# Kernel optimization log

Hardware: AMD Instinct MI355X
Metric: run time of the kernel (lower is better)

Reference implementation:

```python
import jax, jax.numpy as jnp
import numpy as np
from jax import lax

TAU = 0.25
N_TIMESTEPS = 12
OUTPUT_TICKS = 4
INPUT_DIM = 1024
HIDDEN = 1024
OUTPUT_DIM = 1024
CLEANUP = 512
BATCH = 1024
W_SD = 0.1


def setup_inputs() -> dict:
    key = jax.random.key(0)
    ks = jax.random.split(key, 6)
    inputs = jax.random.normal(ks[0], (BATCH, N_TIMESTEPS, INPUT_DIM), dtype=jnp.float32)
    w_oh = W_SD * jax.random.normal(ks[1], (INPUT_DIM, HIDDEN), dtype=jnp.float32)
    w_hp = W_SD * jax.random.normal(ks[2], (HIDDEN, OUTPUT_DIM), dtype=jnp.float32)
    w_pp = W_SD * jax.random.normal(ks[3], (OUTPUT_DIM, OUTPUT_DIM), dtype=jnp.float32)
    w_pc = W_SD * jax.random.normal(ks[4], (OUTPUT_DIM, CLEANUP), dtype=jnp.float32)
    w_cp = W_SD * jax.random.normal(ks[5], (CLEANUP, OUTPUT_DIM), dtype=jnp.float32)
    bias_h = jnp.zeros((HIDDEN,), jnp.float32)
    bias_p = jnp.zeros((OUTPUT_DIM,), jnp.float32)
    bias_c = jnp.zeros((CLEANUP,), jnp.float32)
    return {"inputs": inputs, "w_oh": w_oh, "w_hp": w_hp, "w_pp": w_pp,
            "w_pc": w_pc, "w_cp": w_cp, "bias_h": bias_h, "bias_p": bias_p,
            "bias_c": bias_c}


def reference(inputs, w_oh, w_hp, w_pp, w_pc, w_cp, bias_h, bias_p, bias_c):
    B = inputs.shape[0]
    act = jax.nn.sigmoid
    # time-major input stream: step t consumes o_input[:, t-1, :]
    x = jnp.swapaxes(inputs, 0, 1)  # [T, B, I]

    in_h0 = jnp.zeros((B, HIDDEN), jnp.float32)
    in_p0 = jnp.zeros((B, OUTPUT_DIM), jnp.float32)
    in_c0 = jnp.zeros((B, CLEANUP), jnp.float32)
    carry0 = (in_h0, in_p0, in_c0, in_h0 + 0.5, in_p0 + 0.5, in_c0 + 0.5)

    def step(carry, o_t):
        in_h, in_p, in_c, a_h, a_p, a_c = carry
        # leaky-integrator blends; hp/pp/cp/pc all use PREVIOUS step activations
        h = TAU * (o_t @ w_oh + bias_h) + (1.0 - TAU) * in_h
        p = TAU * (a_h @ w_hp + a_p @ w_pp + a_c @ w_cp + bias_p) + (1.0 - TAU) * in_p
        c = TAU * (a_p @ w_pc + bias_c) + (1.0 - TAU) * in_c
        a_p_new = act(p)
        new_carry = (h, p, c, act(h), a_p_new, act(c))
        return new_carry, a_p_new

    _, act_p_seq = lax.scan(step, carry0, x)  # [T, B, OUTPUT_DIM]
    return act_p_seq[-OUTPUT_TICKS:]  # [OUTPUT_TICKS, B, OUTPUT_DIM]
```

## Files before the change

kernel.cpp:

```cpp
#include <hip/hip_runtime.h>
#include <cstdint>
#include <cstddef>


typedef _Float16 half8 __attribute__((ext_vector_type(8)));
typedef float floatx4 __attribute__((ext_vector_type(4)));

__device__ __forceinline__ void async_cp16(const void* g, void* l) {
  __builtin_amdgcn_global_load_lds(
      (const __attribute__((address_space(1))) void*)g,
      (__attribute__((address_space(3))) void*)l, 16, 0, 0);
}

__device__ __forceinline__ float sigmoidf_(float x) {
  return 1.f / (1.f + __expf(-x));
}

__global__ __launch_bounds__(256) void k_transpose(
    const float* __restrict__ src, int K, int N,
    _Float16* __restrict__ dst, int dst_ld, int k_off) {
  __shared__ float tile[64][65];
  const int k0 = blockIdx.y * 64, n0 = blockIdx.x * 64;
  const int tx = threadIdx.x & 63, ty = threadIdx.x >> 6;
#pragma unroll
  for (int j = 0; j < 16; ++j) {
    int kr = j * 4 + ty;
    tile[kr][tx] = src[(size_t)(k0 + kr) * N + n0 + tx];
  }
  __syncthreads();
#pragma unroll
  for (int j = 0; j < 16; ++j) {
    int nr = j * 4 + ty;
    dst[(size_t)(n0 + nr) * dst_ld + k_off + k0 + tx] = (_Float16)tile[tx][nr];
  }
}

__global__ __launch_bounds__(256) void k_pack_frag(
    const float* __restrict__ src, int N, _Float16* __restrict__ dst,
    int kStride, int kOffChunks) {
  __shared__ float tile[64][65];
  const int k0 = blockIdx.y * 64, n0 = blockIdx.x * 64;
  const int tx = threadIdx.x & 63, ty = threadIdx.x >> 6;
#pragma unroll
  for (int jj = 0; jj < 16; ++jj) {
    int kr = jj * 4 + ty;
    tile[kr][tx] = src[(size_t)(k0 + kr) * N + n0 + tx];
  }
  __syncthreads();
  const int j = threadIdx.x >> 6, lane = threadIdx.x & 63;
  const int r16 = lane & 15, quad = lane >> 4;
#pragma unroll
  for (int c = 0; c < 2; ++c) {
    half8 v;
#pragma unroll
    for (int u = 0; u < 8; ++u)
      v[u] = (_Float16)tile[c * 32 + quad * 8 + u][j * 16 + r16];
    const int kcG = kOffChunks + blockIdx.y * 2 + c;
    *(half8*)(dst + ((size_t)(blockIdx.x * kStride + kcG) * 4 + j) * 512 +
              lane * 8) = v;
  }
}

__global__ __launch_bounds__(256) void k_prep(
    const float* __restrict__ x, _Float16* __restrict__ U,
    _Float16* __restrict__ AH0, _Float16* __restrict__ AP0,
    _Float16* __restrict__ AC0, float* __restrict__ Pst,
    float* __restrict__ Cst) {
  const int id = blockIdx.x * 256 + threadIdx.x;
  const int b = id >> 10, i = id & 1023;
  const float* xb = x + (size_t)b * 12 * 1024 + i;
  float g = 0.f;
#pragma unroll
  for (int t = 0; t < 11; ++t) {
    g = xb[t * 1024] + 0.75f * g;
    U[(size_t)t * 1048576 + id] = (_Float16)g;
  }
  AH0[id] = (_Float16)0.5f;
  AP0[id] = (_Float16)0.5f;
  Pst[id] = 0.f;
  if (i < 512) {
    const int cid = b * 512 + i;
    AC0[cid] = (_Float16)0.5f;
    Cst[cid] = 0.f;
  }
}

__global__ __launch_bounds__(64) void k_gemm_big(
    const _Float16* __restrict__ A, const _Float16* __restrict__ B,
    const float* __restrict__ bias, _Float16* __restrict__ dst, int mode) {
  __shared__ __align__(16) _Float16 sA[2 * 4096];
  __shared__ __align__(16) _Float16 sB[2 * 4096];
  const int lane = threadIdx.x;
  const int mBase = blockIdx.y * 64, nBase = blockIdx.x * 64;
  const int r16 = lane & 15, quad = lane >> 4, mrow = lane >> 3;
  const int gsw = ((lane & 7) ^ (mrow & 7)) * 8;
  const floatx4 zero = {0.f, 0.f, 0.f, 0.f};
  floatx4 acc[4][4];
#pragma unroll
  for (int i = 0; i < 4; ++i)
#pragma unroll
    for (int j = 0; j < 4; ++j) acc[i][j] = zero;

  const _Float16* Abase = A + (size_t)(mBase + mrow) * 1024 + gsw;
  const _Float16* Bbase = B + (size_t)(nBase + mrow) * 1024 + gsw;

  auto stage = [&](int kt, int buf) {
    const int k0 = kt << 6;
#pragma unroll
    for (int q = 0; q < 8; ++q)
      async_cp16(Abase + (size_t)q * 8192 + k0, sA + buf * 4096 + q * 512);
#pragma unroll
    for (int q = 0; q < 8; ++q)
      async_cp16(Bbase + (size_t)q * 8192 + k0, sB + buf * 4096 + q * 512);
  };

  stage(0, 0);
  for (int kt = 0; kt < 16; ++kt) {
    if (kt + 1 < 16) {
      stage(kt + 1, (kt + 1) & 1);
      asm volatile("s_waitcnt vmcnt(16)" ::: "memory");
    } else {
      asm volatile("s_waitcnt vmcnt(0)" ::: "memory");
    }
    const _Float16* sa = sA + (kt & 1) * 4096;
    const _Float16* sb = sB + (kt & 1) * 4096;
#pragma unroll
    for (int kk = 0; kk < 2; ++kk) {
      const int sw = ((kk * 4 + quad) ^ (r16 & 7)) * 8;
      half8 af[4], bf[4];
#pragma unroll
      for (int i = 0; i < 4; ++i) af[i] = *(const half8*)&sa[(i * 16 + r16) * 64 + sw];
#pragma unroll
      for (int j = 0; j < 4; ++j) bf[j] = *(const half8*)&sb[(j * 16 + r16) * 64 + sw];
#pragma unroll
      for (int i = 0; i < 4; ++i)
#pragma unroll
        for (int j = 0; j < 4; ++j)
          acc[i][j] =
              __builtin_amdgcn_mfma_f32_16x16x32_f16(af[i], bf[j], acc[i][j], 0, 0, 0);
    }
  }

  if (mode == 0) {
    const int tm1 = mBase >> 10;
    const float beta = 1.f - __powf(0.75f, (float)(tm1 + 1));
    _Float16* o = dst + (size_t)(mBase + 1024) * 1024;
#pragma unroll
    for (int i = 0; i < 4; ++i)
#pragma unroll
      for (int j = 0; j < 4; ++j) {
        const int n = nBase + j * 16 + r16;
#pragma unroll
        for (int r = 0; r < 4; ++r) {
          const int row = i * 16 + quad * 4 + r;
          const float h = 0.25f * acc[i][j][r] + beta * bias[n];
          o[(size_t)row * 1024 + n] = (_Float16)sigmoidf_(h);
        }
      }
  } else {
    _Float16* o = dst + (size_t)mBase * 1024;
#pragma unroll
    for (int i = 0; i < 4; ++i)
#pragma unroll
      for (int j = 0; j < 4; ++j) {
        const int n = nBase + j * 16 + r16;
#pragma unroll
        for (int r = 0; r < 4; ++r) {
          const int row = i * 16 + quad * 4 + r;
          o[(size_t)row * 1024 + n] = (_Float16)(0.25f * (acc[i][j][r] + bias[n]));
        }
      }
  }
}

__global__ __launch_bounds__(256, 3) void k_step(
    const _Float16* __restrict__ Qt, const _Float16* __restrict__ APc,
    const _Float16* __restrict__ ACc, _Float16* __restrict__ APn,
    _Float16* __restrict__ ACn, const _Float16* __restrict__ Wrf,
    const _Float16* __restrict__ Wcf, const float* __restrict__ bias_c,
    float* __restrict__ Pst, float* __restrict__ Cst,
    float* __restrict__ out_t) {
  __shared__ float red[4][2][4][4][64];
  const int lane = threadIdx.x & 63, w = threadIdx.x >> 6;
  const int r16 = lane & 15, quad = lane >> 4;
  const int blk = blockIdx.x;
  const bool isP = blk < 512;
  int mBase, nt;
  if (isP) {
    mBase = (blk >> 4) * 32;
    nt = blk & 15;
  } else {
    const int b = blk - 512;
    mBase = (b >> 3) * 32;
    nt = b & 7;
  }
  const int nBase = nt * 64;
  const floatx4 zero = {0.f, 0.f, 0.f, 0.f};
  floatx4 acc[2][4];
#pragma unroll
  for (int i = 0; i < 2; ++i)
#pragma unroll
    for (int j = 0; j < 4; ++j) acc[i][j] = zero;

  half8 abuf[3][2], bbuf[3][4];
  auto MM = [&](half8* af, half8* bf) {
#pragma unroll
    for (int i = 0; i < 2; ++i)
#pragma unroll
      for (int j = 0; j < 4; ++j)
        acc[i][j] = __builtin_amdgcn_mfma_f32_16x16x32_f16(af[i], bf[j],
                                                           acc[i][j], 0, 0, 0);
  };

  if (isP) {
    const int kcBase = w * 12;
    auto LD = [&](half8* af, half8* bf, int c) {
      const int kc = kcBase + c;
      const int kg = kc * 32;
      if (kc < 32) {
#pragma unroll
        for (int i = 0; i < 2; ++i)
          af[i] = *(const half8*)(APc + (size_t)(mBase + i * 16 + r16) * 1024 +
                                  kg + quad * 8);
      } else {
#pragma unroll
        for (int i = 0; i < 2; ++i)
          af[i] = *(const half8*)(ACc + (size_t)(mBase + i * 16 + r16) * 512 +
                                  (kg - 1024) + quad * 8);
      }
      const _Float16* wp = Wrf + (size_t)(nt * 48 + kc) * 2048 + lane * 8;
#pragma unroll
      for (int j = 0; j < 4; ++j) bf[j] = *(const half8*)(wp + j * 512);
    };
    LD(abuf[0], bbuf[0], 0);
    LD(abuf[1], bbuf[1], 1);
#pragma unroll
    for (int c = 0; c < 12; ++c) {
      if (c + 2 < 12) LD(abuf[(c + 2) % 3], bbuf[(c + 2) % 3], c + 2);
      MM(abuf[c % 3], bbuf[c % 3]);
    }
  } else {
    const int kcBase = w * 8;
    auto LD = [&](half8* af, half8* bf, int c) {
      const int kc = kcBase + c;
      const int kg = kc * 32;
#pragma unroll
      for (int i = 0; i < 2; ++i)
        af[i] = *(const half8*)(APc + (size_t)(mBase + i * 16 + r16) * 1024 +
                                kg + quad * 8);
      const _Float16* wp = Wcf + (size_t)(nt * 32 + kc) * 2048 + lane * 8;
#pragma unroll
      for (int j = 0; j < 4; ++j) bf[j] = *(const half8*)(wp + j * 512);
    };
    LD(abuf[0], bbuf[0], 0);
    LD(abuf[1], bbuf[1], 1);
#pragma unroll
    for (int c = 0; c < 8; ++c) {
      if (c + 2 < 8) LD(abuf[(c + 2) % 3], bbuf[(c + 2) % 3], c + 2);
      MM(abuf[c % 3], bbuf[c % 3]);
    }
  }

#pragma unroll
  for (int i = 0; i < 2; ++i)
#pragma unroll
    for (int j = 0; j < 4; ++j)
#pragma unroll
      for (int r = 0; r < 4; ++r) red[w][i][j][r][lane] = acc[i][j][r];
  __syncthreads();

  if (isP) {
#pragma unroll
    for (int i = 0; i < 2; ++i) {
      const int n = nBase + w * 16 + r16;
#pragma unroll
      for (int r = 0; r < 4; ++r) {
        const float v = red[0][i][w][r][lane] + red[1][i][w][r][lane] +
                        red[2][i][w][r][lane] + red[3][i][w][r][lane];
        const int b = mBase + i * 16 + quad * 4 + r;
        const size_t o = (size_t)b * 1024 + n;
        const float pn = 0.25f * v + (float)Qt[o] + 0.75f * Pst[o];
        Pst[o] = pn;
        const float a = sigmoidf_(pn);
        APn[o] = (_Float16)a;
        if (out_t) out_t[o] = a;
      }
    }
  } else {
#pragma unroll
    for (int i = 0; i < 2; ++i) {
      const int n = nBase + w * 16 + r16;
#pragma unroll
      for (int r = 0; r < 4; ++r) {
        const float v = red[0][i][w][r][lane] + red[1][i][w][r][lane] +
                        red[2][i][w][r][lane] + red[3][i][w][r][lane];
        const int b = mBase + i * 16 + quad * 4 + r;
        const size_t o = (size_t)b * 512 + n;
        const float cn = 0.25f * (v + bias_c[n]) + 0.75f * Cst[o];
        Cst[o] = cn;
        ACn[o] = (_Float16)sigmoidf_(cn);
      }
    }
  }
}

extern "C" void kernel_launch(void* const* d_in, const int* in_sizes, int n_in,
                              void* d_out, int out_size, void* d_ws,
                              size_t ws_size, hipStream_t stream) {
  const float* x      = (const float*)d_in[0];
  const float* w_oh   = (const float*)d_in[1];
  const float* w_hp   = (const float*)d_in[2];
  const float* w_pp   = (const float*)d_in[3];
  const float* w_pc   = (const float*)d_in[4];
  const float* w_cp   = (const float*)d_in[5];
  const float* bias_h = (const float*)d_in[6];
  const float* bias_p = (const float*)d_in[7];
  const float* bias_c = (const float*)d_in[8];
  float* out = (float*)d_out;

  uint8_t* p = (uint8_t*)d_ws;
  _Float16* Wrf  = (_Float16*)p; p += (size_t)1024 * 1536 * 2;
  _Float16* Wcf  = (_Float16*)p; p += (size_t)512 * 1024 * 2;
  _Float16* WohT = (_Float16*)p; p += (size_t)1024 * 1024 * 2;
  _Float16* Whp  = (_Float16*)p; p += (size_t)1024 * 1024 * 2;
  _Float16* U    = (_Float16*)p; p += (size_t)11 * 1048576 * 2;
  _Float16* AH   = (_Float16*)p; p += (size_t)12 * 1048576 * 2;
  _Float16* Q    = (_Float16*)p; p += (size_t)12 * 1048576 * 2;
  _Float16* AP0  = (_Float16*)p; p += (size_t)1048576 * 2;
  _Float16* AP1  = (_Float16*)p; p += (size_t)1048576 * 2;
  _Float16* AC0  = (_Float16*)p; p += (size_t)512 * 1024 * 2;
  _Float16* AC1  = (_Float16*)p; p += (size_t)512 * 1024 * 2;
  float* Pst = (float*)p; p += (size_t)1048576 * 4;
  float* Cst = (float*)p; p += (size_t)512 * 1024 * 4;

  const dim3 blk256(256);
  k_transpose<<<dim3(16, 16), blk256, 0, stream>>>(w_oh, 1024, 1024, WohT, 1024, 0);
  k_transpose<<<dim3(16, 16), blk256, 0, stream>>>(w_hp, 1024, 1024, Whp, 1024, 0);
  k_pack_frag<<<dim3(16, 16), blk256, 0, stream>>>(w_pp, 1024, Wrf, 48, 0);
  k_pack_frag<<<dim3(16, 8),  blk256, 0, stream>>>(w_cp, 1024, Wrf, 48, 32);
  k_pack_frag<<<dim3(8, 16),  blk256, 0, stream>>>(w_pc, 512, Wcf, 32, 0);
  k_prep<<<4096, blk256, 0, stream>>>(x, U, AH, AP0, AC0, Pst, Cst);
  k_gemm_big<<<dim3(16, 176), dim3(64), 0, stream>>>(U, WohT, bias_h, AH, 0);
  k_gemm_big<<<dim3(16, 192), dim3(64), 0, stream>>>(AH, Whp, bias_p, Q, 1);
  for (int t = 0; t < 12; ++t) {
    const _Float16* APc = (t & 1) ? AP1 : AP0;
    _Float16* APn       = (t & 1) ? AP0 : AP1;
    const _Float16* ACc = (t & 1) ? AC1 : AC0;
    _Float16* ACn       = (t & 1) ? AC0 : AC1;
    float* ot = (t >= 8) ? out + (size_t)(t - 8) * 1048576 : (float*)nullptr;
    k_step<<<dim3(768), blk256, 0, stream>>>(Q + (size_t)t * 1048576, APc,
                                             ACc, APn, ACn, Wrf, Wcf, bias_c,
                                             Pst, Cst, ot);
  }
}
```

Before: 435.9 us.

## Use 128x128 four-wave tiles in big GEMM with cooperative LDS staging

The batched input and hidden-to-output GEMMs move from a single-wave 64x64 tile to a 256-thread block computing a 128x128 tile, with four waves sharing the A and B tiles in LDS. This halves global loads per output and cuts block count fourfold. The double-buffered async prefetch is dropped for a single buffer with a full vmcnt wait and two barriers per k-step, so load latency is no longer hidden behind MFMA work.

```diff
diff --git a/kernel.cpp b/kernel.cpp
--- a/kernel.cpp
+++ b/kernel.cpp
@@ -85,15 +85,19 @@
   }
 }
 
-__global__ __launch_bounds__(64) void k_gemm_big(
+__global__ __launch_bounds__(256, 3) void k_gemm_big(
     const _Float16* __restrict__ A, const _Float16* __restrict__ B,
     const float* __restrict__ bias, _Float16* __restrict__ dst, int mode) {
-  __shared__ __align__(16) _Float16 sA[2 * 4096];
-  __shared__ __align__(16) _Float16 sB[2 * 4096];
-  const int lane = threadIdx.x;
-  const int mBase = blockIdx.y * 64, nBase = blockIdx.x * 64;
-  const int r16 = lane & 15, quad = lane >> 4, mrow = lane >> 3;
-  const int gsw = ((lane & 7) ^ (mrow & 7)) * 8;
+  __shared__ __align__(16) _Float16 sA[128 * 64];
+  __shared__ __align__(16) _Float16 sB[128 * 64];
+  const int tid = threadIdx.x;
+  const int lane = tid & 63, w = tid >> 6;
+  const int mBase = blockIdx.y * 128, nBase = blockIdx.x * 128;
+  const int r16 = lane & 15, quad = lane >> 4;
+  const int lrow = lane >> 3;
+  const int gsw = ((lane & 7) ^ lrow) * 8;
+  const int wr = w >> 1, wc = w & 1;
+
   const floatx4 zero = {0.f, 0.f, 0.f, 0.f};
   floatx4 acc[4][4];
 #pragma unroll
@@ -101,44 +105,41 @@
 #pragma unroll
     for (int j = 0; j < 4; ++j) acc[i][j] = zero;
 
-  const _Float16* Abase = A + (size_t)(mBase + mrow) * 1024 + gsw;
-  const _Float16* Bbase = B + (size_t)(nBase + mrow) * 1024 + gsw;
-
-  auto stage = [&](int kt, int buf) {
+  const _Float16* Abase = A + (size_t)(mBase + w * 32 + lrow) * 1024 + gsw;
+  const _Float16* Bbase = B + (size_t)(nBase + w * 32 + lrow) * 1024 + gsw;
+  _Float16* sAw = sA + (w * 32) * 64;
+  _Float16* sBw = sB + (w * 32) * 64;
+  const _Float16* sa = sA + (size_t)wr * 64 * 64;
+  const _Float16* sb = sB + (size_t)wc * 64 * 64;
+
+  for (int kt = 0; kt < 16; ++kt) {
     const int k0 = kt << 6;
 #pragma unroll
-    for (int q = 0; q < 8; ++q)
-      async_cp16(Abase + (size_t)q * 8192 + k0, sA + buf * 4096 + q * 512);
-#pragma unroll
-    for (int q = 0; q < 8; ++q)
-      async_cp16(Bbase + (size_t)q * 8192 + k0, sB + buf * 4096 + q * 512);
-  };
-
-  stage(0, 0);
-  for (int kt = 0; kt < 16; ++kt) {
-    if (kt + 1 < 16) {
-      stage(kt + 1, (kt + 1) & 1);
-      asm volatile("s_waitcnt vmcnt(16)" ::: "memory");
-    } else {
-      asm volatile("s_waitcnt vmcnt(0)" ::: "memory");
-    }
-    const _Float16* sa = sA + (kt & 1) * 4096;
-    const _Float16* sb = sB + (kt & 1) * 4096;
+    for (int q = 0; q < 4; ++q)
+      async_cp16(Abase + (size_t)q * 8192 + k0, sAw + q * 512);
+#pragma unroll
+    for (int q = 0; q < 4; ++q)
+      async_cp16(Bbase + (size_t)q * 8192 + k0, sBw + q * 512);
+    asm volatile("s_waitcnt vmcnt(0)" ::: "memory");
+    __syncthreads();
 #pragma unroll
     for (int kk = 0; kk < 2; ++kk) {
       const int sw = ((kk * 4 + quad) ^ (r16 & 7)) * 8;
       half8 af[4], bf[4];
 #pragma unroll
-      for (int i = 0; i < 4; ++i) af[i] = *(const half8*)&sa[(i * 16 + r16) * 64 + sw];
-#pragma unroll
-      for (int j = 0; j < 4; ++j) bf[j] = *(const half8*)&sb[(j * 16 + r16) * 64 + sw];
-#pragma unroll
       for (int i = 0; i < 4; ++i)
+        af[i] = *(const half8*)&sa[(i * 16 + r16) * 64 + sw];
+#pragma unroll
+      for (int j = 0; j < 4; ++j)
+        bf[j] = *(const half8*)&sb[(j * 16 + r16) * 64 + sw];
+#pragma unroll
+      for (int i = 0; i < 4; ++i)
 #pragma unroll
         for (int j = 0; j < 4; ++j)
-          acc[i][j] =
-              __builtin_amdgcn_mfma_f32_16x16x32_f16(af[i], bf[j], acc[i][j], 0, 0, 0);
-    }
+          acc[i][j] = __builtin_amdgcn_mfma_f32_16x16x32_f16(af[i], bf[j],
+                                                             acc[i][j], 0, 0, 0);
+    }
+    __syncthreads();
   }
 
   if (mode == 0) {
@@ -149,10 +150,10 @@
     for (int i = 0; i < 4; ++i)
 #pragma unroll
       for (int j = 0; j < 4; ++j) {
-        const int n = nBase + j * 16 + r16;
+        const int n = nBase + wc * 64 + j * 16 + r16;
 #pragma unroll
         for (int r = 0; r < 4; ++r) {
-          const int row = i * 16 + quad * 4 + r;
+          const int row = wr * 64 + i * 16 + quad * 4 + r;
           const float h = 0.25f * acc[i][j][r] + beta * bias[n];
           o[(size_t)row * 1024 + n] = (_Float16)sigmoidf_(h);
         }
@@ -163,10 +164,10 @@
     for (int i = 0; i < 4; ++i)
 #pragma unroll
       for (int j = 0; j < 4; ++j) {
-        const int n = nBase + j * 16 + r16;
+        const int n = nBase + wc * 64 + j * 16 + r16;
 #pragma unroll
         for (int r = 0; r < 4; ++r) {
-          const int row = i * 16 + quad * 4 + r;
+          const int row = wr * 64 + i * 16 + quad * 4 + r;
           o[(size_t)row * 1024 + n] = (_Float16)(0.25f * (acc[i][j][r] + bias[n]));
         }
       }
@@ -340,8 +341,8 @@
   k_pack_frag<<<dim3(16, 8),  blk256, 0, stream>>>(w_cp, 1024, Wrf, 48, 32);
   k_pack_frag<<<dim3(8, 16),  blk256, 0, stream>>>(w_pc, 512, Wcf, 32, 0);
   k_prep<<<4096, blk256, 0, stream>>>(x, U, AH, AP0, AC0, Pst, Cst);
-  k_gemm_big<<<dim3(16, 176), dim3(64), 0, stream>>>(U, WohT, bias_h, AH, 0);
-  k_gemm_big<<<dim3(16, 192), dim3(64), 0, stream>>>(AH, Whp, bias_p, Q, 1);
+  k_gemm_big<<<dim3(8, 88), blk256, 0, stream>>>(U, WohT, bias_h, AH, 0);
+  k_gemm_big<<<dim3(8, 96), blk256, 0, stream>>>(AH, Whp, bias_p, Q, 1);
   for (int t = 0; t < 12; ++t) {
     const _Float16* APc = (t & 1) ? AP1 : AP0;
     _Float16* APn       = (t & 1) ? AP0 : AP1;
```

New measurement: 395.0 us. 9.4% less time.
